# Kernel optimization log

Measured on AMD Instinct MI355X. Metric: run time of the kernel, lower is better.

Reference implementation:

```python
import jax, jax.numpy as jnp
import numpy as np

HEIGHT = 8  # output crop height (module init arg)


def setup_inputs() -> dict:
    key = jax.random.key(0)
    k = jax.random.split(key, 8)
    N, Himg, Wimg, C = 16, 512, 512, 3
    M = 8192  # total boxes across the batch
    images = jax.random.normal(k[0], (N, Himg, Wimg, C), jnp.float32)
    feature_map = jax.random.normal(k[1], (N, 128, 128, 32), jnp.float32)
    # boxes: (x1, y1, x2, y2, angle); sized so width = HEIGHT*bw/bh <= 60 < max_width=64
    x1 = jax.random.uniform(k[2], (M,), minval=0.0, maxval=392.0)
    y1 = jax.random.uniform(k[3], (M,), minval=0.0, maxval=448.0)
    bw = jax.random.uniform(k[4], (M,), minval=16.0, maxval=120.0)
    bh = jax.random.uniform(k[5], (M,), minval=16.0, maxval=64.0)
    ang = jax.random.uniform(k[6], (M,), minval=-0.785, maxval=0.785)
    boxes = jnp.stack([x1, y1, x1 + bw, y1 + bh, ang], axis=-1)
    box_indices = jax.random.randint(k[7], (M,), 0, N).astype(jnp.int32)
    return {"images": images, "feature_map": feature_map, "boxes": boxes,
            "box_indices": box_indices, "max_width": 64}


def _roi_rotate(images, boxes, box_indices, max_width):
    """Rotated crop-and-resize with bilinear sampling.
    Returns crops [M, HEIGHT, max_width, C] (zero-padded past each box's width)
    and the per-box float output widths [M]."""
    Himg, Wimg = images.shape[1], images.shape[2]
    x1, y1, x2, y2, ang = (boxes[:, i] for i in range(5))
    bw, bh = x2 - x1, y2 - y1
    width = HEIGHT * bw / bh                      # per-box output width (float)
    cx, cy = (x1 + x2) * 0.5, (y1 + y2) * 0.5     # box center
    s = (bh / HEIGHT)[:, None, None]              # uniform scale (src px per dst px)

    ii = jnp.arange(HEIGHT, dtype=images.dtype)[None, :, None]      # [1,H,1]
    jj = jnp.arange(max_width, dtype=images.dtype)[None, None, :]   # [1,1,W]
    w_ = width[:, None, None]
    dx = s * (jj - (w_ - 1.0) * 0.5)              # [M,H,W] local offsets
    dy = s * (ii - (HEIGHT - 1.0) * 0.5)
    ca = jnp.cos(ang)[:, None, None]
    sa = jnp.sin(ang)[:, None, None]
    sx = cx[:, None, None] + ca * dx - sa * dy    # rotated source coords
    sy = cy[:, None, None] + sa * dx + ca * dy

    x0 = jnp.floor(sx)
    y0 = jnp.floor(sy)
    fx = (sx - x0)[..., None]
    fy = (sy - y0)[..., None]
    x0i = jnp.clip(x0, 0, Wimg - 1).astype(jnp.int32)
    x1i = jnp.clip(x0 + 1.0, 0, Wimg - 1).astype(jnp.int32)
    y0i = jnp.clip(y0, 0, Himg - 1).astype(jnp.int32)
    y1i = jnp.clip(y0 + 1.0, 0, Himg - 1).astype(jnp.int32)

    b = box_indices[:, None, None]                # [M,1,1] broadcasts to [M,H,W]
    v00 = images[b, y0i, x0i]                     # [M,H,W,C] irregular gathers
    v01 = images[b, y0i, x1i]
    v10 = images[b, y1i, x0i]
    v11 = images[b, y1i, x1i]
    out = (v00 * (1 - fx) * (1 - fy) + v01 * fx * (1 - fy)
           + v10 * (1 - fx) * fy + v11 * fx * fy)

    # zero outside the image and past each box's actual width (padding)
    valid = ((jj < jnp.ceil(w_)) & (sx >= 0) & (sx <= Wimg - 1)
             & (sy >= 0) & (sy <= Himg - 1))
    crops = out * valid[..., None].astype(out.dtype)
    return crops, width


def reference(images, feature_map, boxes, box_indices, max_width):
    # feature_map is accepted (forward signature) but, per the source, crops
    # are taken from `images`.
    crops, width = _roi_rotate(images, boxes, box_indices, max_width)
    boxes_padded_width = max_width - width
    return crops, boxes_padded_width
```

## Files before the change

kernel.cpp:

```cpp
#include <hip/hip_runtime.h>

#define HEIGHT 8

__global__ void __launch_bounds__(512)
roi_rotate_kernel(const float* __restrict__ images,
                  const float* __restrict__ boxes,
                  const int* __restrict__ box_indices,
                  float* __restrict__ crops,
                  float* __restrict__ width_out,
                  int max_width, int Himg, int Wimg)
{
    const int m   = blockIdx.x;
    const int tid = threadIdx.x;
    const int mw  = max_width;
    const int i   = tid / mw;
    const int j   = tid - i * mw;

    const float x1  = boxes[m * 5 + 0];
    const float y1  = boxes[m * 5 + 1];
    const float x2  = boxes[m * 5 + 2];
    const float y2  = boxes[m * 5 + 3];
    const float ang = boxes[m * 5 + 4];
    const float bwd = x2 - x1, bhd = y2 - y1;
    const float width = (float)HEIGHT * bwd / bhd;
    const float cx = (x1 + x2) * 0.5f;
    const float cy = (y1 + y2) * 0.5f;
    const float s  = bhd / (float)HEIGHT;
    const float ca = cosf(ang);
    const float sa = sinf(ang);
    if (tid == 0) width_out[m] = (float)mw - width;

    const float dx = s * ((float)j - (width - 1.0f) * 0.5f);
    const float dy = s * ((float)i - ((float)HEIGHT - 1.0f) * 0.5f);
    const float sx = cx + ca * dx - sa * dy;
    const float sy = cy + sa * dx + ca * dy;

    float v0 = 0.0f, v1 = 0.0f, v2 = 0.0f;

    const bool valid = ((float)j < ceilf(width)) &&
                       (sx >= 0.0f) && (sx <= (float)(Wimg - 1)) &&
                       (sy >= 0.0f) && (sy <= (float)(Himg - 1));

    if (valid) {
        const float x0 = floorf(sx);
        const float y0 = floorf(sy);
        const int x0i = (int)x0;
        const int y0i = (int)y0;

        const int xb = min(x0i, Wimg - 2);
        const int yb = min(y0i, Himg - 2);
        const float fx = (x0i == xb) ? (sx - x0) : 1.0f;
        const float fy = (y0i == yb) ? (sy - y0) : 1.0f;

        const int b = box_indices[m];
        const float* img = images + (size_t)b * Himg * Wimg * 3;
        const float* r0 = img + ((size_t)yb * Wimg + xb) * 3;
        const float* r1 = r0 + (size_t)Wimg * 3;

        float s0[6], s1[6];
        __builtin_memcpy(s0, r0, 24);
        __builtin_memcpy(s1, r1, 24);

        const float w00 = (1.0f - fx) * (1.0f - fy);
        const float w01 = fx * (1.0f - fy);
        const float w10 = (1.0f - fx) * fy;
        const float w11 = fx * fy;

        v0 = s0[0] * w00 + s0[3] * w01 + s1[0] * w10 + s1[3] * w11;
        v1 = s0[1] * w00 + s0[4] * w01 + s1[1] * w10 + s1[4] * w11;
        v2 = s0[2] * w00 + s0[5] * w01 + s1[2] * w10 + s1[5] * w11;
    }

    float* o = crops + ((size_t)(m * HEIGHT + i) * mw + j) * 3;
    o[0] = v0; o[1] = v1; o[2] = v2;
}

extern "C" void kernel_launch(void* const* d_in, const int* in_sizes, int n_in,
                              void* d_out, int out_size, void* d_ws, size_t ws_size,
                              hipStream_t stream) {
    const float* images      = (const float*)d_in[0];
    const float* boxes       = (const float*)d_in[2];
    const int*   box_indices = (const int*)d_in[3];

    const int M  = in_sizes[3];
    const int mw = (out_size - M) / (M * HEIGHT * 3);
    const int Himg = 512, Wimg = 512;

    float* crops     = (float*)d_out;
    float* width_out = crops + (size_t)M * HEIGHT * mw * 3;

    dim3 block(HEIGHT * mw);
    dim3 grid(M);
    roi_rotate_kernel<<<grid, block, 0, stream>>>(images, boxes, box_indices,
                                                  crops, width_out, mw, Himg, Wimg);
}
```

Measured before the change: 37.12 us.

## Bucket boxes by image index onto XCDs for L2 locality

Splits the work into three kernels: one precomputes per-box parameters, one single-block kernel groups boxes by image index modulo 8, and a persistent main kernel whose blocks, assigned round-robin by blockIdx, each process only boxes from one group. The intent is that each XCD's L2 serves gathers from only two of the sixteen images, reducing cache misses on the irregular bilinear reads. It adds two extra launches, a serial single-block bucketing pass, and a fixed 1024-block grid that may balance load unevenly. It also assumes block-to-XCD dispatch is round-robin.

```diff
diff --git a/kernel.cpp b/kernel.cpp
--- a/kernel.cpp
+++ b/kernel.cpp
@@ -1,21 +1,17 @@
 #include <hip/hip_runtime.h>
 
 #define HEIGHT 8
+#define NXCD 8
 
-__global__ void __launch_bounds__(512)
-roi_rotate_kernel(const float* __restrict__ images,
-                  const float* __restrict__ boxes,
+__global__ void __launch_bounds__(256)
+box_params_kernel(const float* __restrict__ boxes,
                   const int* __restrict__ box_indices,
-                  float* __restrict__ crops,
+                  float4* __restrict__ params,
                   float* __restrict__ width_out,
-                  int max_width, int Himg, int Wimg)
+                  int M, int mw)
 {
-    const int m   = blockIdx.x;
-    const int tid = threadIdx.x;
-    const int mw  = max_width;
-    const int i   = tid / mw;
-    const int j   = tid - i * mw;
-
+    int m = blockIdx.x * blockDim.x + threadIdx.x;
+    if (m >= M) return;
     const float x1  = boxes[m * 5 + 0];
     const float y1  = boxes[m * 5 + 1];
     const float x2  = boxes[m * 5 + 2];
@@ -23,56 +19,134 @@
     const float ang = boxes[m * 5 + 4];
     const float bwd = x2 - x1, bhd = y2 - y1;
     const float width = (float)HEIGHT * bwd / bhd;
-    const float cx = (x1 + x2) * 0.5f;
-    const float cy = (y1 + y2) * 0.5f;
-    const float s  = bhd / (float)HEIGHT;
-    const float ca = cosf(ang);
-    const float sa = sinf(ang);
-    if (tid == 0) width_out[m] = (float)mw - width;
+    params[2 * m]     = make_float4((x1 + x2) * 0.5f, (y1 + y2) * 0.5f,
+                                    bhd / (float)HEIGHT, width);
+    params[2 * m + 1] = make_float4(cosf(ang), sinf(ang), ceilf(width),
+                                    __int_as_float(box_indices[m]));
+    width_out[m] = (float)mw - width;
+}
 
-    const float dx = s * ((float)j - (width - 1.0f) * 0.5f);
-    const float dy = s * ((float)i - ((float)HEIGHT - 1.0f) * 0.5f);
-    const float sx = cx + ca * dx - sa * dy;
-    const float sy = cy + sa * dx + ca * dy;
+__global__ void __launch_bounds__(1024)
+bucket_kernel(const int* __restrict__ box_indices,
+              int* __restrict__ perm,
+              int* __restrict__ off_g,
+              int M)
+{
+    __shared__ int h[NXCD];
+    __shared__ int base[NXCD];
+    const int t    = threadIdx.x;
+    const int lane = t & 63;
+    if (t < NXCD) h[t] = 0;
+    __syncthreads();
 
-    float v0 = 0.0f, v1 = 0.0f, v2 = 0.0f;
+    for (int m = t; m < M; m += blockDim.x) {
+        const int g = box_indices[m] & (NXCD - 1);
+        #pragma unroll
+        for (int q = 0; q < NXCD; ++q) {
+            const unsigned long long mask = __ballot(g == q);
+            if (g == q) {
+                const int leader = __ffsll((unsigned long long)mask) - 1;
+                if (lane == leader) atomicAdd(&h[q], __popcll(mask));
+            }
+        }
+    }
+    __syncthreads();
 
-    const bool valid = ((float)j < ceilf(width)) &&
-                       (sx >= 0.0f) && (sx <= (float)(Wimg - 1)) &&
-                       (sy >= 0.0f) && (sy <= (float)(Himg - 1));
+    if (t == 0) {
+        int acc = 0;
+        #pragma unroll
+        for (int q = 0; q < NXCD; ++q) { base[q] = acc; off_g[q] = acc; acc += h[q]; }
+        off_g[NXCD] = acc;
+    }
+    __syncthreads();
 
-    if (valid) {
-        const float x0 = floorf(sx);
-        const float y0 = floorf(sy);
-        const int x0i = (int)x0;
-        const int y0i = (int)y0;
+    for (int m = t; m < M; m += blockDim.x) {
+        const int g = box_indices[m] & (NXCD - 1);
+        #pragma unroll
+        for (int q = 0; q < NXCD; ++q) {
+            const unsigned long long mask = __ballot(g == q);
+            if (g == q) {
+                const unsigned long long lt = (1ull << lane) - 1ull;
+                const int rank   = __popcll(mask & lt);
+                const int leader = __ffsll((unsigned long long)mask) - 1;
+                int wb = 0;
+                if (lane == leader) wb = atomicAdd(&base[q], __popcll(mask));
+                wb = __shfl(wb, leader, 64);
+                perm[wb + rank] = m;
+            }
+        }
+    }
+}
 
-        const int xb = min(x0i, Wimg - 2);
-        const int yb = min(y0i, Himg - 2);
-        const float fx = (x0i == xb) ? (sx - x0) : 1.0f;
-        const float fy = (y0i == yb) ? (sy - y0) : 1.0f;
+__global__ void __launch_bounds__(512)
+roi_main_kernel(const float* __restrict__ images,
+                const float4* __restrict__ params,
+                const int* __restrict__ perm,
+                const int* __restrict__ off_g,
+                float* __restrict__ crops,
+                int mw, int Himg, int Wimg)
+{
+    const int x   = blockIdx.x & (NXCD - 1);
+    const int r   = blockIdx.x >> 3;
+    const int nb  = (int)gridDim.x >> 3;
+    const int tid = threadIdx.x;
+    const int pbeg = off_g[x];
+    const int pend = off_g[x + 1];
+    const int nsamp = HEIGHT * mw;
 
-        const int b = box_indices[m];
+    for (int p = pbeg + r; p < pend; p += nb) {
+        const int m = perm[p];
+        const float4 pA = params[2 * m];
+        const float4 pB = params[2 * m + 1];
+        const float cx = pA.x, cy = pA.y, s = pA.z, width = pA.w;
+        const float ca = pB.x, sa = pB.y, wlim = pB.z;
+        const int   b  = __float_as_int(pB.w);
         const float* img = images + (size_t)b * Himg * Wimg * 3;
-        const float* r0 = img + ((size_t)yb * Wimg + xb) * 3;
-        const float* r1 = r0 + (size_t)Wimg * 3;
+        float* oblk = crops + (size_t)m * nsamp * 3;
 
-        float s0[6], s1[6];
-        __builtin_memcpy(s0, r0, 24);
-        __builtin_memcpy(s1, r1, 24);
+        for (int idx = tid; idx < nsamp; idx += blockDim.x) {
+            int i, j;
+            if (mw == 64) { i = idx >> 6; j = idx & 63; }
+            else          { i = idx / mw; j = idx - i * mw; }
 
-        const float w00 = (1.0f - fx) * (1.0f - fy);
-        const float w01 = fx * (1.0f - fy);
-        const float w10 = (1.0f - fx) * fy;
-        const float w11 = fx * fy;
+            const float dx = s * ((float)j - (width - 1.0f) * 0.5f);
+            const float dy = s * ((float)i - ((float)HEIGHT - 1.0f) * 0.5f);
+            const float sx = cx + ca * dx - sa * dy;
+            const float sy = cy + sa * dx + ca * dy;
 
-        v0 = s0[0] * w00 + s0[3] * w01 + s1[0] * w10 + s1[3] * w11;
-        v1 = s0[1] * w00 + s0[4] * w01 + s1[1] * w10 + s1[4] * w11;
-        v2 = s0[2] * w00 + s0[5] * w01 + s1[2] * w10 + s1[5] * w11;
+            float v0 = 0.0f, v1 = 0.0f, v2 = 0.0f;
+            const bool valid = ((float)j < wlim) &&
+                               (sx >= 0.0f) && (sx <= (float)(Wimg - 1)) &&
+                               (sy >= 0.0f) && (sy <= (float)(Himg - 1));
+            if (valid) {
+                const float x0 = floorf(sx);
+                const float y0 = floorf(sy);
+                const int x0i = (int)x0;
+                const int y0i = (int)y0;
+                const int xb  = min(x0i, Wimg - 2);
+                const int yb  = min(y0i, Himg - 2);
+                const float fx = (x0i == xb) ? (sx - x0) : 1.0f;
+                const float fy = (y0i == yb) ? (sy - y0) : 1.0f;
+
+                const float* r0 = img + ((size_t)yb * Wimg + xb) * 3;
+                const float* r1 = r0 + (size_t)Wimg * 3;
+                float s0[6], s1[6];
+                __builtin_memcpy(s0, r0, 24);
+                __builtin_memcpy(s1, r1, 24);
+
+                const float w00 = (1.0f - fx) * (1.0f - fy);
+                const float w01 = fx * (1.0f - fy);
+                const float w10 = (1.0f - fx) * fy;
+                const float w11 = fx * fy;
+
+                v0 = s0[0] * w00 + s0[3] * w01 + s1[0] * w10 + s1[3] * w11;
+                v1 = s0[1] * w00 + s0[4] * w01 + s1[1] * w10 + s1[4] * w11;
+                v2 = s0[2] * w00 + s0[5] * w01 + s1[2] * w10 + s1[5] * w11;
+            }
+            float* o = oblk + (size_t)idx * 3;
+            o[0] = v0; o[1] = v1; o[2] = v2;
+        }
     }
-
-    float* o = crops + ((size_t)(m * HEIGHT + i) * mw + j) * 3;
-    o[0] = v0; o[1] = v1; o[2] = v2;
 }
 
 extern "C" void kernel_launch(void* const* d_in, const int* in_sizes, int n_in,
@@ -89,8 +163,13 @@
     float* crops     = (float*)d_out;
     float* width_out = crops + (size_t)M * HEIGHT * mw * 3;
 
-    dim3 block(HEIGHT * mw);
-    dim3 grid(M);
-    roi_rotate_kernel<<<grid, block, 0, stream>>>(images, boxes, box_indices,
-                                                  crops, width_out, mw, Himg, Wimg);
+    float4* params = (float4*)d_ws;
+    int*    perm   = (int*)((char*)d_ws + (size_t)2 * M * sizeof(float4));
+    int*    off_g  = perm + M;
+
+    box_params_kernel<<<(M + 255) / 256, 256, 0, stream>>>(
+        boxes, box_indices, params, width_out, M, mw);
+    bucket_kernel<<<1, 1024, 0, stream>>>(box_indices, perm, off_g, M);
+    roi_main_kernel<<<1024, 512, 0, stream>>>(
+        images, params, perm, off_g, crops, mw, Himg, Wimg);
 }
```

Result: slower. 55.53 us (+49.6%).

## Precompute box params, prefetch images into cache, use nontemporal crop stores

Applied to the files above, without the earlier changes.

Splits the work into a prep kernel that computes per-box center, scale, trig and width into a workspace, a prefetch kernel that streams the entire image tensor to warm the last-level cache, and a main gather kernel. The main kernel stores crops with nontemporal stores to avoid polluting the cache. The intent is to make the irregular bilinear gathers hit cache. The cost is a full extra read of the image tensor and two additional launches.

```diff
diff --git a/kernel.cpp b/kernel.cpp
--- a/kernel.cpp
+++ b/kernel.cpp
@@ -2,20 +2,15 @@
 
 #define HEIGHT 8
 
-__global__ void __launch_bounds__(512)
-roi_rotate_kernel(const float* __restrict__ images,
-                  const float* __restrict__ boxes,
-                  const int* __restrict__ box_indices,
-                  float* __restrict__ crops,
-                  float* __restrict__ width_out,
-                  int max_width, int Himg, int Wimg)
+__global__ void __launch_bounds__(256)
+prep_kernel(const float* __restrict__ boxes,
+            const int* __restrict__ box_indices,
+            float4* __restrict__ params,
+            float* __restrict__ width_out,
+            int M, int mw)
 {
-    const int m   = blockIdx.x;
-    const int tid = threadIdx.x;
-    const int mw  = max_width;
-    const int i   = tid / mw;
-    const int j   = tid - i * mw;
-
+    const int m = blockIdx.x * 256 + threadIdx.x;
+    if (m >= M) return;
     const float x1  = boxes[m * 5 + 0];
     const float y1  = boxes[m * 5 + 1];
     const float x2  = boxes[m * 5 + 2];
@@ -23,21 +18,50 @@
     const float ang = boxes[m * 5 + 4];
     const float bwd = x2 - x1, bhd = y2 - y1;
     const float width = (float)HEIGHT * bwd / bhd;
-    const float cx = (x1 + x2) * 0.5f;
-    const float cy = (y1 + y2) * 0.5f;
-    const float s  = bhd / (float)HEIGHT;
-    const float ca = cosf(ang);
-    const float sa = sinf(ang);
-    if (tid == 0) width_out[m] = (float)mw - width;
+    params[2 * m]     = make_float4((x1 + x2) * 0.5f, (y1 + y2) * 0.5f,
+                                    bhd / (float)HEIGHT, (width - 1.0f) * 0.5f);
+    params[2 * m + 1] = make_float4(cosf(ang), sinf(ang), ceilf(width),
+                                    __int_as_float(box_indices[m]));
+    width_out[m] = (float)mw - width;
+}
 
-    const float dx = s * ((float)j - (width - 1.0f) * 0.5f);
+__global__ void __launch_bounds__(256)
+prefetch_kernel(const float4* __restrict__ imgs, unsigned long long n4)
+{
+    float acc = 0.0f;
+    const unsigned long long stride = (unsigned long long)gridDim.x * 256ull;
+    for (unsigned long long i = blockIdx.x * 256ull + threadIdx.x; i < n4; i += stride) {
+        const float4 v = imgs[i];
+        acc += v.x + v.y + v.z + v.w;
+    }
+    asm volatile("" :: "v"(acc));
+}
+
+__global__ void __launch_bounds__(512)
+roi_main_kernel(const float* __restrict__ images,
+                const float4* __restrict__ params,
+                float* __restrict__ crops,
+                int mw, int Himg, int Wimg)
+{
+    const int m   = blockIdx.x;
+    const int tid = threadIdx.x;
+    const int i   = tid / mw;
+    const int j   = tid - i * mw;
+
+    const float4 pA = params[2 * m];
+    const float4 pB = params[2 * m + 1];
+    const float cx = pA.x, cy = pA.y, s = pA.z, px = pA.w;
+    const float ca = pB.x, sa = pB.y, wlim = pB.z;
+    const int   b  = __float_as_int(pB.w);
+
+    const float dx = s * ((float)j - px);
     const float dy = s * ((float)i - ((float)HEIGHT - 1.0f) * 0.5f);
     const float sx = cx + ca * dx - sa * dy;
     const float sy = cy + sa * dx + ca * dy;
 
     float v0 = 0.0f, v1 = 0.0f, v2 = 0.0f;
 
-    const bool valid = ((float)j < ceilf(width)) &&
+    const bool valid = ((float)j < wlim) &&
                        (sx >= 0.0f) && (sx <= (float)(Wimg - 1)) &&
                        (sy >= 0.0f) && (sy <= (float)(Himg - 1));
 
@@ -46,17 +70,14 @@
         const float y0 = floorf(sy);
         const int x0i = (int)x0;
         const int y0i = (int)y0;
-
-        const int xb = min(x0i, Wimg - 2);
-        const int yb = min(y0i, Himg - 2);
+        const int xb  = min(x0i, Wimg - 2);
+        const int yb  = min(y0i, Himg - 2);
         const float fx = (x0i == xb) ? (sx - x0) : 1.0f;
         const float fy = (y0i == yb) ? (sy - y0) : 1.0f;
 
-        const int b = box_indices[m];
         const float* img = images + (size_t)b * Himg * Wimg * 3;
-        const float* r0 = img + ((size_t)yb * Wimg + xb) * 3;
-        const float* r1 = r0 + (size_t)Wimg * 3;
-
+        const float* r0  = img + ((size_t)yb * Wimg + xb) * 3;
+        const float* r1  = r0 + (size_t)Wimg * 3;
         float s0[6], s1[6];
         __builtin_memcpy(s0, r0, 24);
         __builtin_memcpy(s1, r1, 24);
@@ -72,7 +93,9 @@
     }
 
     float* o = crops + ((size_t)(m * HEIGHT + i) * mw + j) * 3;
-    o[0] = v0; o[1] = v1; o[2] = v2;
+    __builtin_nontemporal_store(v0, o + 0);
+    __builtin_nontemporal_store(v1, o + 1);
+    __builtin_nontemporal_store(v2, o + 2);
 }
 
 extern "C" void kernel_launch(void* const* d_in, const int* in_sizes, int n_in,
@@ -89,8 +112,14 @@
     float* crops     = (float*)d_out;
     float* width_out = crops + (size_t)M * HEIGHT * mw * 3;
 
-    dim3 block(HEIGHT * mw);
-    dim3 grid(M);
-    roi_rotate_kernel<<<grid, block, 0, stream>>>(images, boxes, box_indices,
-                                                  crops, width_out, mw, Himg, Wimg);
+    float4* params = (float4*)d_ws;
+
+    prep_kernel<<<(M + 255) / 256, 256, 0, stream>>>(
+        boxes, box_indices, params, width_out, M, mw);
+
+    const unsigned long long n4 = (unsigned long long)in_sizes[0] / 4;
+    prefetch_kernel<<<2048, 256, 0, stream>>>((const float4*)images, n4);
+
+    roi_main_kernel<<<M, HEIGHT * mw, 0, stream>>>(
+        images, params, crops, mw, Himg, Wimg);
 }
```

Measured after the change: 49.09 us. +32.2%, slower.
